# Optimization experiments

Measured on AMD Instinct MI355X. Metric: run time of the kernel, lower is better.

The kernel has to match this reference:

```python
import jax, jax.numpy as jnp
import numpy as np

N, E, D, NUM_REL, NUM_LAYERS = 20000, 100000, 768, 7, 5  # 6 edge types + self-loop relation


def setup_inputs() -> dict:
    key = jax.random.key(0)
    ks = jax.random.split(key, 8)
    x = jax.random.normal(ks[0], (N, D), dtype=jnp.float32)
    edge_index = jax.random.randint(ks[1], (2, E), 0, N, dtype=jnp.int64)
    # original edge_type values are in [-1, 5]; module adds 1 -> [0, 6]
    edge_type = jax.random.randint(ks[2], (E,), -1, 6, dtype=jnp.int64)
    scale = 1.0 / np.sqrt(D)
    weights = jax.random.normal(ks[3], (NUM_LAYERS, NUM_REL, D, D), dtype=jnp.float32) * scale
    roots = jax.random.normal(ks[4], (NUM_LAYERS, D, D), dtype=jnp.float32) * scale
    biases = jax.random.normal(ks[5], (NUM_LAYERS, D), dtype=jnp.float32) * 0.01
    return {"x": x, "edge_index": edge_index, "edge_type": edge_type,
            "weights": weights, "roots": roots, "biases": biases}


def _rgcn_conv(h, src, dst, safe_et, W, root, b):
    # PyG RGCNConv (aggr='mean', root_weight=True, bias=True):
    #   out = x @ root + b + sum_r mean_{edges of rel r into v}(x[src]) @ W_r
    n = h.shape[0]
    hs = h[src]  # [E, D] gather once, reused across relations
    out = h @ root + b
    for r in range(NUM_REL):
        m = (safe_et == r).astype(h.dtype)  # [E]
        msg_sum = jax.ops.segment_sum(hs * m[:, None], dst, num_segments=n)  # [N, D]
        cnt = jax.ops.segment_sum(m, dst, num_segments=n)  # [N]
        mean = msg_sum / jnp.maximum(cnt, 1.0)[:, None]  # zero where no rel-r edges
        out = out + mean @ W[r]
    return out


def reference(x, edge_index, edge_type, weights, roots, biases):
    src, dst = edge_index[0], edge_index[1]
    safe_et = edge_type + 1  # [-1..5] -> [0..6]
    h = x
    for l in range(NUM_LAYERS):
        h = _rgcn_conv(h, src, dst, safe_et, weights[l], roots[l], biases[l])
        h = jax.nn.relu(h)  # dropout=0 -> identity
    return h
```

## Files before the change

kernel.cpp:

```cpp
#include <hip/hip_runtime.h>

typedef unsigned short u16;
typedef unsigned int   u32;
typedef __attribute__((ext_vector_type(8))) short short8;
typedef __attribute__((ext_vector_type(4))) float f32x4;

#define DD      768
#define KK      6144
#define NREL    7
#define NLAYERS 5

__device__ __forceinline__ float b2f(u16 v) {
  return __uint_as_float(((u32)v) << 16);
}
__device__ __forceinline__ u16 f2bf(float f) {
  u32 x = __float_as_uint(f);
  x += 0x7fffu + ((x >> 16) & 1u);
  return (u16)(x >> 16);
}
__device__ __forceinline__ void gload16(const void* g, void* l) {
  __builtin_amdgcn_global_load_lds(
      (const __attribute__((address_space(1))) void*)g,
      (__attribute__((address_space(3))) void*)l, 16, 0, 0);
}


__global__ void cast_x_kernel(const float* __restrict__ x, u16* __restrict__ H, size_t n) {
  for (size_t i = ((size_t)blockIdx.x * 256 + threadIdx.x) * 4; i < n; i += (size_t)gridDim.x * 256 * 4) {
    float4 v = *(const float4*)&x[i];
    u32 lo = (u32)f2bf(v.x) | ((u32)f2bf(v.y) << 16);
    u32 hi = (u32)f2bf(v.z) | ((u32)f2bf(v.w) << 16);
    uint2 o; o.x = lo; o.y = hi;
    *(uint2*)&H[i] = o;
  }
}

__global__ void count_kernel(const int* __restrict__ eidx, const int* __restrict__ etype,
                             int* cnt_dst, int* cnt_rel, int E, int Nn) {
  int e = blockIdx.x * 256 + threadIdx.x;
  if (e >= E) return;
  int dst = eidx[E + e];
  int rel = etype[e] + 1;
  atomicAdd(&cnt_dst[dst], 1);
  atomicAdd(&cnt_rel[(size_t)rel * Nn + dst], 1);
}

__global__ __launch_bounds__(1024) void scan_kernel(const int* __restrict__ cnt, int* __restrict__ offs, int n) {
  __shared__ int part[1024];
  int t = threadIdx.x;
  int per = (n + 1023) / 1024;
  int base = t * per;
  int s = 0;
  for (int i = 0; i < per; ++i) { int idx = base + i; if (idx < n) s += cnt[idx]; }
  part[t] = s;
  __syncthreads();
  for (int o = 1; o < 1024; o <<= 1) {
    int v = (t >= o) ? part[t - o] : 0;
    __syncthreads();
    part[t] += v;
    __syncthreads();
  }
  int excl = (t == 0) ? 0 : part[t - 1];
  s = excl;
  for (int i = 0; i < per; ++i) { int idx = base + i; if (idx < n) { offs[idx] = s; s += cnt[idx]; } }
  if (t == 1023) offs[n] = part[1023];
}

__global__ void fillperm_kernel(const int* __restrict__ eidx, const int* __restrict__ offs,
                                int* fill, int* perm, int E) {
  int e = blockIdx.x * 256 + threadIdx.x;
  if (e >= E) return;
  int dst = eidx[E + e];
  int pos = offs[dst] + atomicAdd(&fill[dst], 1);
  perm[pos] = e;
}

__global__ void wcat_kernel(const float* __restrict__ W, const float* __restrict__ R, u16* __restrict__ Bt) {
  __shared__ float t[32 * 33];
  int b = blockIdx.x;
  int s = b / 576, rem = b % 576;
  int kt = rem / 24, nt = rem % 24;
  const float* src = (s == 0) ? R : (W + (size_t)(s - 1) * DD * DD);
  int tj = threadIdx.x & 31, ti = threadIdx.x >> 5;
#pragma unroll
  for (int i = 0; i < 4; ++i) {
    int kk = kt * 32 + ti + i * 8;
    t[(ti + i * 8) * 33 + tj] = src[(size_t)kk * DD + nt * 32 + tj];
  }
  __syncthreads();
#pragma unroll
  for (int i = 0; i < 4; ++i) {
    int nn_ = nt * 32 + ti + i * 8;
    Bt[(size_t)nn_ * KK + (size_t)s * DD + kt * 32 + tj] = f2bf(t[tj * 33 + ti + i * 8]);
  }
}

__global__ __launch_bounds__(192) void aggregate_kernel(
    const u16* __restrict__ H, const int* __restrict__ esrc, const int* __restrict__ etype,
    const int* __restrict__ offs, const int* __restrict__ perm, const int* __restrict__ cnt_rel,
    u16* __restrict__ Acat, int node0, int Nn) {
  int v = node0 + blockIdx.x;
  int t = threadIdx.x;
  int j0 = t * 4;
  size_t rowbase = (size_t)blockIdx.x * KK;
  *(uint2*)&Acat[rowbase + j0] = *(const uint2*)&H[(size_t)v * DD + j0];
  float a0[4] = {0,0,0,0}, a1[4] = {0,0,0,0}, a2[4] = {0,0,0,0}, a3[4] = {0,0,0,0};
  float a4[4] = {0,0,0,0}, a5[4] = {0,0,0,0}, a6[4] = {0,0,0,0};
  int beg = offs[v], end = offs[v + 1];
  for (int e = beg; e < end; ++e) {
    int eid = perm[e];
    int src = esrc[eid];
    int rel = etype[eid] + 1;
    uint2 w = *(const uint2*)&H[(size_t)src * DD + j0];
    float f0 = b2f((u16)(w.x & 0xffff));
    float f1 = b2f((u16)(w.x >> 16));
    float f2 = b2f((u16)(w.y & 0xffff));
    float f3 = b2f((u16)(w.y >> 16));
    switch (rel) {
      case 0: a0[0]+=f0; a0[1]+=f1; a0[2]+=f2; a0[3]+=f3; break;
      case 1: a1[0]+=f0; a1[1]+=f1; a1[2]+=f2; a1[3]+=f3; break;
      case 2: a2[0]+=f0; a2[1]+=f1; a2[2]+=f2; a2[3]+=f3; break;
      case 3: a3[0]+=f0; a3[1]+=f1; a3[2]+=f2; a3[3]+=f3; break;
      case 4: a4[0]+=f0; a4[1]+=f1; a4[2]+=f2; a4[3]+=f3; break;
      case 5: a5[0]+=f0; a5[1]+=f1; a5[2]+=f2; a5[3]+=f3; break;
      default: a6[0]+=f0; a6[1]+=f1; a6[2]+=f2; a6[3]+=f3; break;
    }
  }
  const float* regs[NREL] = {a0, a1, a2, a3, a4, a5, a6};
#pragma unroll
  for (int r = 0; r < NREL; ++r) {
    int c = cnt_rel[(size_t)r * Nn + v];
    float inv = (c > 0) ? 1.f / (float)c : 0.f;
    const float* a = regs[r];
    u32 lo = (u32)f2bf(a[0] * inv) | ((u32)f2bf(a[1] * inv) << 16);
    u32 hi = (u32)f2bf(a[2] * inv) | ((u32)f2bf(a[3] * inv) << 16);
    uint2 o; o.x = lo; o.y = hi;
    *(uint2*)&Acat[rowbase + (size_t)(r + 1) * DD + j0] = o;
  }
}


#define MFMA_(a_, b_, c_) __builtin_amdgcn_mfma_f32_16x16x32_bf16(a_, b_, c_, 0, 0, 0)

__global__ __launch_bounds__(512, 4) void gemm128_kernel(
    const u16* __restrict__ A, const u16* __restrict__ Bt, const float* __restrict__ bias,
    u16* __restrict__ Hout, float* __restrict__ Cout, int Mvalid, int Mtiles) {
  __shared__ u16 smA[3][128 * 32];
  __shared__ u16 smB[3][256 * 32];

  int tid = threadIdx.x;
  int lane = tid & 63;
  int wv = tid >> 6;
  int wm = wv >> 2, wn = wv & 3;

  int nwg = Mtiles * 3;
  int orig = (int)blockIdx.x;
  int q8 = nwg >> 3, r8 = nwg & 7;
  int xcd = orig & 7, rank = orig >> 3;
  int wg = (xcd < r8 ? xcd * (q8 + 1) : r8 * (q8 + 1) + (xcd - r8) * q8) + rank;
  int bm = wg / 3, bn = wg % 3;

  int srow = tid >> 2;
  int schunk = (tid & 3) ^ ((tid >> 3) & 3);
  int ra = bm * 128 + srow; if (ra > Mvalid - 1) ra = Mvalid - 1;
  const char* gA  = (const char*)A  + (size_t)ra * (KK * 2) + schunk * 16;
  const char* gB0 = (const char*)Bt + (size_t)(bn * 256 + srow) * (KK * 2) + schunk * 16;
  const char* gB1 = gB0 + (size_t)128 * (KK * 2);

  int rsel = lane & 15, kq = lane >> 4;
  int loff = rsel * 64 + ((kq ^ ((rsel >> 1) & 3)) * 16);

  f32x4 acc[4][4];
#pragma unroll
  for (int m = 0; m < 4; ++m)
#pragma unroll
    for (int n = 0; n < 4; ++n) acc[m][n] = (f32x4){0.f, 0.f, 0.f, 0.f};

  const int NSTEP = KK / 32;

#define STAGE(t2, slot)                                                  \
  do {                                                                   \
    size_t ko_ = (size_t)(t2) * 64;                                      \
    gload16(gA + ko_,  (char*)&smA[slot][0] + tid * 16);                 \
    gload16(gB0 + ko_, (char*)&smB[slot][0] + tid * 16);                 \
    gload16(gB1 + ko_, (char*)&smB[slot][0] + 8192 + tid * 16);          \
  } while (0)

#define KSTEP(tt, cur, nxt)                                              \
  do {                                                                   \
    if ((tt) + 2 < NSTEP) STAGE((tt) + 2, nxt);                          \
    const char* aB_ = (const char*)&smA[cur][0] + wm * 4096 + loff;      \
    const char* bB_ = (const char*)&smB[cur][0] + wn * 4096 + loff;      \
    short8 af_[4], bf_[4];                                               \
    _Pragma("unroll")                                                    \
    for (int m_ = 0; m_ < 4; ++m_) af_[m_] = *(const short8*)(aB_ + m_ * 1024); \
    _Pragma("unroll")                                                    \
    for (int n_ = 0; n_ < 4; ++n_) bf_[n_] = *(const short8*)(bB_ + n_ * 1024); \
    __builtin_amdgcn_s_setprio(1);                                       \
    _Pragma("unroll")                                                    \
    for (int m_ = 0; m_ < 4; ++m_)                                       \
      _Pragma("unroll")                                                  \
      for (int n_ = 0; n_ < 4; ++n_)                                     \
        acc[m_][n_] = MFMA_(af_[m_], bf_[n_], acc[m_][n_]);              \
    __builtin_amdgcn_s_setprio(0);                                       \
    if ((tt) + 2 < NSTEP) asm volatile("s_waitcnt vmcnt(3)" ::: "memory"); \
    else                  asm volatile("s_waitcnt vmcnt(0)" ::: "memory"); \
    __builtin_amdgcn_s_barrier();                                        \
  } while (0)

  STAGE(0, 0);
  STAGE(1, 1);
  asm volatile("s_waitcnt vmcnt(3)" ::: "memory");
  __builtin_amdgcn_s_barrier();

  for (int t = 0; t < NSTEP; t += 3) {
    KSTEP(t,     0, 2);
    KSTEP(t + 1, 1, 0);
    KSTEP(t + 2, 2, 1);
  }
#undef KSTEP
#undef STAGE

  int rif = (lane >> 4) * 4;
  int cidx = lane & 15;
#pragma unroll
  for (int m = 0; m < 4; ++m) {
    int rl = bm * 128 + wm * 64 + m * 16 + rif;
#pragma unroll
    for (int n = 0; n < 4; ++n) {
      int c = bn * 256 + wn * 64 + n * 16 + cidx;
      float bv = bias[c];
#pragma unroll
      for (int j = 0; j < 4; ++j) {
        int r = rl + j;
        if (r < Mvalid) {
          float v = acc[m][n][j] + bv;
          v = v > 0.f ? v : 0.f;
          if (Hout) Hout[(size_t)r * DD + c] = f2bf(v);
          if (Cout) Cout[(size_t)r * DD + c] = v;
        }
      }
    }
  }
}


static inline size_t alignup(size_t x, size_t a) { return (x + a - 1) & ~(a - 1); }

extern "C" void kernel_launch(void* const* d_in, const int* in_sizes, int n_in,
                              void* d_out, int out_size, void* d_ws, size_t ws_size,
                              hipStream_t stream) {
  const float* x       = (const float*)d_in[0];
  const int*   eidx    = (const int*)d_in[1];
  const int*   etype   = (const int*)d_in[2];
  const float* weights = (const float*)d_in[3];
  const float* roots   = (const float*)d_in[4];
  const float* biases  = (const float*)d_in[5];
  float* out = (float*)d_out;

  const int Nn = in_sizes[0] / DD;
  const int E  = in_sizes[2];

  char* p = (char*)d_ws;
  size_t off = 0;
  auto carve = [&](size_t bytes) -> char* {
    char* r = p + off;
    off = alignup(off + bytes, 256);
    return r;
  };
  u16* H0      = (u16*)carve((size_t)Nn * DD * 2);
  u16* Bt      = (u16*)carve((size_t)DD * KK * 2);
  int* cnt_rel = (int*)carve((size_t)NREL * Nn * 4);
  int* cnt_dst = (int*)carve((size_t)Nn * 4);
  int* offs    = (int*)carve((size_t)(Nn + 1) * 4);
  int* fill    = (int*)carve((size_t)Nn * 4);
  int* perm    = (int*)carve((size_t)E * 4);

  size_t rem = (ws_size > off) ? (ws_size - off) : 0;
  int McCap = (int)(rem / ((size_t)KK * 2));
  int Mpad = ((Nn + 127) / 128) * 128;
  int Mc = (McCap < Mpad) ? (McCap & ~127) : Mpad;
  if (Mc < 128) return;
  u16* Acat = (u16*)(p + off);
  int nchunks = (Nn + Mc - 1) / Mc;
  u16* H1 = (u16*)d_out;

  (void)hipMemsetAsync(cnt_rel, 0, (size_t)NREL * Nn * 4, stream);
  (void)hipMemsetAsync(cnt_dst, 0, (size_t)Nn * 4, stream);
  (void)hipMemsetAsync(fill, 0, (size_t)Nn * 4, stream);

  int eg = (E + 255) / 256;
  count_kernel<<<eg, 256, 0, stream>>>(eidx, etype, cnt_dst, cnt_rel, E, Nn);
  scan_kernel<<<1, 1024, 0, stream>>>(cnt_dst, offs, Nn);
  fillperm_kernel<<<eg, 256, 0, stream>>>(eidx, offs, fill, perm, E);
  cast_x_kernel<<<2048, 256, 0, stream>>>(x, H0, (size_t)Nn * DD);

  const u16* Hin = H0;
  u16* Hnext = H1;
  for (int l = 0; l < NLAYERS; ++l) {
    wcat_kernel<<<8 * 576, 256, 0, stream>>>(weights + (size_t)l * NREL * DD * DD,
                                             roots + (size_t)l * DD * DD, Bt);
    for (int c = 0; c < nchunks; ++c) {
      int node0 = c * Mc;
      int nn = (Nn - node0 < Mc) ? (Nn - node0) : Mc;
      aggregate_kernel<<<nn, 192, 0, stream>>>(Hin, eidx, etype, offs, perm, cnt_rel,
                                               Acat, node0, Nn);
      int mt = (nn + 127) / 128;
      u16* ho = (l < NLAYERS - 1) ? (Hnext + (size_t)node0 * DD) : nullptr;
      float* co = (l == NLAYERS - 1) ? (out + (size_t)node0 * DD) : nullptr;
      gemm128_kernel<<<mt * 3, 512, 0, stream>>>(Acat, Bt, biases + (size_t)l * DD, ho, co, nn, mt);
    }
    const u16* t_ = Hin;
    Hin = Hnext;
    Hnext = (u16*)t_;
  }
}
```

Measured before the change: 1.583 ms.

## Pre-tile A and B into MFMA fragment layout and load fragments directly without LDS

Result: slower. 2.423 ms (+53.1%).

```diff
diff --git a/kernel.cpp b/kernel.cpp
--- a/kernel.cpp
+++ b/kernel.cpp
@@ -9,6 +9,7 @@
 #define KK      6144
 #define NREL    7
 #define NLAYERS 5
+#define TILEB   196608
 
 __device__ __forceinline__ float b2f(u16 v) {
   return __uint_as_float(((u32)v) << 16);
@@ -17,11 +18,6 @@
   u32 x = __float_as_uint(f);
   x += 0x7fffu + ((x >> 16) & 1u);
   return (u16)(x >> 16);
-}
-__device__ __forceinline__ void gload16(const void* g, void* l) {
-  __builtin_amdgcn_global_load_lds(
-      (const __attribute__((address_space(1))) void*)g,
-      (__attribute__((address_space(3))) void*)l, 16, 0, 0);
 }
 
 
@@ -75,7 +71,7 @@
   perm[pos] = e;
 }
 
-__global__ void wcat_kernel(const float* __restrict__ W, const float* __restrict__ R, u16* __restrict__ Bt) {
+__global__ void wcat_kernel(const float* __restrict__ W, const float* __restrict__ R, u16* __restrict__ Bn) {
   __shared__ float t[32 * 33];
   int b = blockIdx.x;
   int s = b / 576, rem = b % 576;
@@ -88,27 +84,35 @@
     t[(ti + i * 8) * 33 + tj] = src[(size_t)kk * DD + nt * 32 + tj];
   }
   __syncthreads();
+  int kkidx = s * 24 + kt;
+  int kq = tj >> 3, e = tj & 7;
 #pragma unroll
   for (int i = 0; i < 4; ++i) {
-    int nn_ = nt * 32 + ti + i * 8;
-    Bt[(size_t)nn_ * KK + (size_t)s * DD + kt * 32 + tj] = f2bf(t[tj * 33 + ti + i * 8]);
+    int n = nt * 32 + ti + i * 8;
+    size_t idx = ((size_t)(n >> 4) * 192 + kkidx) * 512 + (size_t)(kq * 16 + (n & 15)) * 8 + e;
+    Bn[idx] = f2bf(t[tj * 33 + ti + i * 8]);
   }
 }
 
 __global__ __launch_bounds__(192) void aggregate_kernel(
     const u16* __restrict__ H, const int* __restrict__ esrc, const int* __restrict__ etype,
     const int* __restrict__ offs, const int* __restrict__ perm, const int* __restrict__ cnt_rel,
-    u16* __restrict__ Acat, int node0, int Nn) {
+    u16* __restrict__ An, int node0, int Nn) {
   int v = node0 + blockIdx.x;
   int t = threadIdx.x;
   int j0 = t * 4;
-  size_t rowbase = (size_t)blockIdx.x * KK;
-  *(uint2*)&Acat[rowbase + j0] = *(const uint2*)&H[(size_t)v * DD + j0];
+  int rr = blockIdx.x;
+  int tile16 = rr >> 4, rsel = rr & 15;
+  int kq = (j0 & 31) >> 3, e = j0 & 7, kk0 = j0 >> 5;
+  size_t base = ((size_t)tile16 * 192 + kk0) * 512 + (size_t)(kq * 16 + rsel) * 8 + e;
+
+  *(uint2*)&An[base] = *(const uint2*)&H[(size_t)v * DD + j0];
+
   float a0[4] = {0,0,0,0}, a1[4] = {0,0,0,0}, a2[4] = {0,0,0,0}, a3[4] = {0,0,0,0};
   float a4[4] = {0,0,0,0}, a5[4] = {0,0,0,0}, a6[4] = {0,0,0,0};
   int beg = offs[v], end = offs[v + 1];
-  for (int e = beg; e < end; ++e) {
-    int eid = perm[e];
+  for (int eI = beg; eI < end; ++eI) {
+    int eid = perm[eI];
     int src = esrc[eid];
     int rel = etype[eid] + 1;
     uint2 w = *(const uint2*)&H[(size_t)src * DD + j0];
@@ -135,100 +139,86 @@
     u32 lo = (u32)f2bf(a[0] * inv) | ((u32)f2bf(a[1] * inv) << 16);
     u32 hi = (u32)f2bf(a[2] * inv) | ((u32)f2bf(a[3] * inv) << 16);
     uint2 o; o.x = lo; o.y = hi;
-    *(uint2*)&Acat[rowbase + (size_t)(r + 1) * DD + j0] = o;
+    *(uint2*)&An[base + (size_t)(r + 1) * 24 * 512] = o;
   }
 }
 
 
 #define MFMA_(a_, b_, c_) __builtin_amdgcn_mfma_f32_16x16x32_bf16(a_, b_, c_, 0, 0, 0)
 
-__global__ __launch_bounds__(512, 4) void gemm128_kernel(
-    const u16* __restrict__ A, const u16* __restrict__ Bt, const float* __restrict__ bias,
+__global__ __launch_bounds__(256, 2) void gemmfl_kernel(
+    const u16* __restrict__ An, const u16* __restrict__ Bn, const float* __restrict__ bias,
     u16* __restrict__ Hout, float* __restrict__ Cout, int Mvalid, int Mtiles) {
-  __shared__ u16 smA[3][128 * 32];
-  __shared__ u16 smB[3][256 * 32];
-
   int tid = threadIdx.x;
   int lane = tid & 63;
   int wv = tid >> 6;
-  int wm = wv >> 2, wn = wv & 3;
 
   int nwg = Mtiles * 3;
   int orig = (int)blockIdx.x;
   int q8 = nwg >> 3, r8 = nwg & 7;
   int xcd = orig & 7, rank = orig >> 3;
   int wg = (xcd < r8 ? xcd * (q8 + 1) : r8 * (q8 + 1) + (xcd - r8) * q8) + rank;
-  int bm = wg / 3, bn = wg % 3;
-
-  int srow = tid >> 2;
-  int schunk = (tid & 3) ^ ((tid >> 3) & 3);
-  int ra = bm * 128 + srow; if (ra > Mvalid - 1) ra = Mvalid - 1;
-  const char* gA  = (const char*)A  + (size_t)ra * (KK * 2) + schunk * 16;
-  const char* gB0 = (const char*)Bt + (size_t)(bn * 256 + srow) * (KK * 2) + schunk * 16;
-  const char* gB1 = gB0 + (size_t)128 * (KK * 2);
-
-  int rsel = lane & 15, kq = lane >> 4;
-  int loff = rsel * 64 + ((kq ^ ((rsel >> 1) & 3)) * 16);
-
-  f32x4 acc[4][4];
-#pragma unroll
-  for (int m = 0; m < 4; ++m)
+  int bm = wg / 3, bq = wg % 3;
+  int nq = bq * 4 + wv;
+
+  const char* pa = (const char*)An + (size_t)(bm * 8) * TILEB;
+  const char* pb = (const char*)Bn + (size_t)(nq * 4) * TILEB;
+  int voff = lane * 16;
+
+  f32x4 acc[8][4];
+#pragma unroll
+  for (int m = 0; m < 8; ++m)
 #pragma unroll
     for (int n = 0; n < 4; ++n) acc[m][n] = (f32x4){0.f, 0.f, 0.f, 0.f};
 
-  const int NSTEP = KK / 32;
-
-#define STAGE(t2, slot)                                                  \
-  do {                                                                   \
-    size_t ko_ = (size_t)(t2) * 64;                                      \
-    gload16(gA + ko_,  (char*)&smA[slot][0] + tid * 16);                 \
-    gload16(gB0 + ko_, (char*)&smB[slot][0] + tid * 16);                 \
-    gload16(gB1 + ko_, (char*)&smB[slot][0] + 8192 + tid * 16);          \
+#define LOADK(kk, ar, br)                                                 \
+  do {                                                                    \
+    int o_ = (kk) * 1024 + voff;                                          \
+    _Pragma("unroll")                                                     \
+    for (int m_ = 0; m_ < 8; ++m_) ar[m_] = *(const short8*)(pa + m_ * TILEB + o_); \
+    _Pragma("unroll")                                                     \
+    for (int n_ = 0; n_ < 4; ++n_) br[n_] = *(const short8*)(pb + n_ * TILEB + o_); \
   } while (0)
 
-#define KSTEP(tt, cur, nxt)                                              \
-  do {                                                                   \
-    if ((tt) + 2 < NSTEP) STAGE((tt) + 2, nxt);                          \
-    const char* aB_ = (const char*)&smA[cur][0] + wm * 4096 + loff;      \
-    const char* bB_ = (const char*)&smB[cur][0] + wn * 4096 + loff;      \
-    short8 af_[4], bf_[4];                                               \
-    _Pragma("unroll")                                                    \
-    for (int m_ = 0; m_ < 4; ++m_) af_[m_] = *(const short8*)(aB_ + m_ * 1024); \
-    _Pragma("unroll")                                                    \
-    for (int n_ = 0; n_ < 4; ++n_) bf_[n_] = *(const short8*)(bB_ + n_ * 1024); \
-    __builtin_amdgcn_s_setprio(1);                                       \
-    _Pragma("unroll")                                                    \
-    for (int m_ = 0; m_ < 4; ++m_)                                       \
-      _Pragma("unroll")                                                  \
-      for (int n_ = 0; n_ < 4; ++n_)                                     \
-        acc[m_][n_] = MFMA_(af_[m_], bf_[n_], acc[m_][n_]);              \
-    __builtin_amdgcn_s_setprio(0);                                       \
-    if ((tt) + 2 < NSTEP) asm volatile("s_waitcnt vmcnt(3)" ::: "memory"); \
-    else                  asm volatile("s_waitcnt vmcnt(0)" ::: "memory"); \
-    __builtin_amdgcn_s_barrier();                                        \
+#define MF32(ar, br)                                                      \
+  do {                                                                    \
+    __builtin_amdgcn_s_setprio(1);                                        \
+    _Pragma("unroll")                                                     \
+    for (int m_ = 0; m_ < 8; ++m_)                                        \
+      _Pragma("unroll")                                                   \
+      for (int n_ = 0; n_ < 4; ++n_)                                      \
+        acc[m_][n_] = MFMA_(ar[m_], br[n_], acc[m_][n_]);                 \
+    __builtin_amdgcn_s_setprio(0);                                        \
   } while (0)
 
-  STAGE(0, 0);
-  STAGE(1, 1);
-  asm volatile("s_waitcnt vmcnt(3)" ::: "memory");
-  __builtin_amdgcn_s_barrier();
-
-  for (int t = 0; t < NSTEP; t += 3) {
-    KSTEP(t,     0, 2);
-    KSTEP(t + 1, 1, 0);
-    KSTEP(t + 2, 2, 1);
-  }
-#undef KSTEP
-#undef STAGE
+  short8 aA[8], bA[4], aB[8], bB[4];
+  LOADK(0, aA, bA);
+  LOADK(1, aB, bB);
+
+  for (int kk = 0; kk < 188; kk += 2) {
+    MF32(aA, bA);
+    LOADK(kk + 2, aA, bA);
+    MF32(aB, bB);
+    LOADK(kk + 3, aB, bB);
+  }
+  MF32(aA, bA);
+  LOADK(190, aA, bA);
+  MF32(aB, bB);
+  LOADK(191, aB, bB);
+  MF32(aA, bA);
+  MF32(aB, bB);
+
+#undef LOADK
+#undef MF32
 
   int rif = (lane >> 4) * 4;
   int cidx = lane & 15;
 #pragma unroll
-  for (int m = 0; m < 4; ++m) {
-    int rl = bm * 128 + wm * 64 + m * 16 + rif;
+  for (int m = 0; m < 8; ++m) {
+    int rl = bm * 128 + m * 16 + rif;
 #pragma unroll
     for (int n = 0; n < 4; ++n) {
-      int c = bn * 256 + wn * 64 + n * 16 + cidx;
+      int c = nq * 64 + n * 16 + cidx;
       float bv = bias[c];
 #pragma unroll
       for (int j = 0; j < 4; ++j) {
@@ -269,7 +259,7 @@
     return r;
   };
   u16* H0      = (u16*)carve((size_t)Nn * DD * 2);
-  u16* Bt      = (u16*)carve((size_t)DD * KK * 2);
+  u16* Bn      = (u16*)carve((size_t)DD * KK * 2);
   int* cnt_rel = (int*)carve((size_t)NREL * Nn * 4);
   int* cnt_dst = (int*)carve((size_t)Nn * 4);
   int* offs    = (int*)carve((size_t)(Nn + 1) * 4);
@@ -281,7 +271,7 @@
   int Mpad = ((Nn + 127) / 128) * 128;
   int Mc = (McCap < Mpad) ? (McCap & ~127) : Mpad;
   if (Mc < 128) return;
-  u16* Acat = (u16*)(p + off);
+  u16* An = (u16*)(p + off);
   int nchunks = (Nn + Mc - 1) / Mc;
   u16* H1 = (u16*)d_out;
 
@@ -299,16 +289,16 @@
   u16* Hnext = H1;
   for (int l = 0; l < NLAYERS; ++l) {
     wcat_kernel<<<8 * 576, 256, 0, stream>>>(weights + (size_t)l * NREL * DD * DD,
-                                             roots + (size_t)l * DD * DD, Bt);
+                                             roots + (size_t)l * DD * DD, Bn);
     for (int c = 0; c < nchunks; ++c) {
       int node0 = c * Mc;
       int nn = (Nn - node0 < Mc) ? (Nn - node0) : Mc;
       aggregate_kernel<<<nn, 192, 0, stream>>>(Hin, eidx, etype, offs, perm, cnt_rel,
-                                               Acat, node0, Nn);
+                                               An, node0, Nn);
       int mt = (nn + 127) / 128;
       u16* ho = (l < NLAYERS - 1) ? (Hnext + (size_t)node0 * DD) : nullptr;
       float* co = (l == NLAYERS - 1) ? (out + (size_t)node0 * DD) : nullptr;
-      gemm128_kernel<<<mt * 3, 512, 0, stream>>>(Acat, Bt, biases + (size_t)l * DD, ho, co, nn, mt);
+      gemmfl_kernel<<<mt * 3, 256, 0, stream>>>(An, Bn, biases + (size_t)l * DD, ho, co, nn, mt);
     }
     const u16* t_ = Hin;
     Hin = Hnext;
```

## Replace GEMM with 256x256-tile eight-phase pipelined MFMA kernel

Applied to the files above, without the earlier changes.

After: 1.430 ms. 9.6% less time.

```diff
diff --git a/kernel.cpp b/kernel.cpp
--- a/kernel.cpp
+++ b/kernel.cpp
@@ -141,12 +141,20 @@
 
 
 #define MFMA_(a_, b_, c_) __builtin_amdgcn_mfma_f32_16x16x32_bf16(a_, b_, c_, 0, 0, 0)
-
-__global__ __launch_bounds__(512, 4) void gemm128_kernel(
+#define BAR   __builtin_amdgcn_s_barrier()
+#define SB    __builtin_amdgcn_sched_barrier(0)
+#define LGKM0 asm volatile("s_waitcnt lgkmcnt(0)" ::: "memory")
+#define VM10  asm volatile("s_waitcnt vmcnt(10)" ::: "memory")
+#define VM8   asm volatile("s_waitcnt vmcnt(8)" ::: "memory")
+#define VM4   asm volatile("s_waitcnt vmcnt(4)" ::: "memory")
+#define VM2   asm volatile("s_waitcnt vmcnt(2)" ::: "memory")
+#define VM0   asm volatile("s_waitcnt vmcnt(0)" ::: "memory")
+
+__global__ __launch_bounds__(512, 2) void gemm8p_kernel(
     const u16* __restrict__ A, const u16* __restrict__ Bt, const float* __restrict__ bias,
     u16* __restrict__ Hout, float* __restrict__ Cout, int Mvalid, int Mtiles) {
-  __shared__ u16 smA[3][128 * 32];
-  __shared__ u16 smB[3][256 * 32];
+  __shared__ char smA[2][2][16384];
+  __shared__ char smB[2][2][16384];
 
   int tid = threadIdx.x;
   int lane = tid & 63;
@@ -160,72 +168,125 @@
   int wg = (xcd < r8 ? xcd * (q8 + 1) : r8 * (q8 + 1) + (xcd - r8) * q8) + rank;
   int bm = wg / 3, bn = wg % 3;
 
-  int srow = tid >> 2;
-  int schunk = (tid & 3) ^ ((tid >> 3) & 3);
-  int ra = bm * 128 + srow; if (ra > Mvalid - 1) ra = Mvalid - 1;
-  const char* gA  = (const char*)A  + (size_t)ra * (KK * 2) + schunk * 16;
-  const char* gB0 = (const char*)Bt + (size_t)(bn * 256 + srow) * (KK * 2) + schunk * 16;
-  const char* gB1 = gB0 + (size_t)128 * (KK * 2);
-
+  const char* pA[2][2];
+  const char* pB[2][2];
+#pragma unroll
+  for (int j = 0; j < 2; ++j) {
+    int q = j * 512 + tid, rl = q >> 3, gc = (q & 7) ^ (rl & 7);
+    int ra0 = (rl & 63) + ((rl >> 6) << 7);
+    int rb0 = (rl & 31) + ((rl >> 5) << 6);
+    pA[0][j] = (const char*)A  + ((size_t)(bm * 256 + ra0) * KK) * 2 + gc * 16;
+    pA[1][j] = pA[0][j] + (size_t)64 * KK * 2;
+    pB[0][j] = (const char*)Bt + ((size_t)(bn * 256 + rb0) * KK) * 2 + gc * 16;
+    pB[1][j] = pB[0][j] + (size_t)32 * KK * 2;
+  }
   int rsel = lane & 15, kq = lane >> 4;
-  int loff = rsel * 64 + ((kq ^ ((rsel >> 1) & 3)) * 16);
-
-  f32x4 acc[4][4];
-#pragma unroll
-  for (int m = 0; m < 4; ++m)
+  int loff0 = rsel * 128 + (((kq)     ^ (rsel & 7)) * 16);
+  int loff1 = rsel * 128 + (((kq + 4) ^ (rsel & 7)) * 16);
+
+  f32x4 acc[8][4];
+#pragma unroll
+  for (int m = 0; m < 8; ++m)
 #pragma unroll
     for (int n = 0; n < 4; ++n) acc[m][n] = (f32x4){0.f, 0.f, 0.f, 0.f};
 
-  const int NSTEP = KK / 32;
-
-#define STAGE(t2, slot)                                                  \
-  do {                                                                   \
-    size_t ko_ = (size_t)(t2) * 64;                                      \
-    gload16(gA + ko_,  (char*)&smA[slot][0] + tid * 16);                 \
-    gload16(gB0 + ko_, (char*)&smB[slot][0] + tid * 16);                 \
-    gload16(gB1 + ko_, (char*)&smB[slot][0] + 8192 + tid * 16);          \
+  short8 a03[4][2], a47[4][2], b01[2][2], b23[2][2];
+
+#define STGA(s_, h_, t2)                                                  \
+  do {                                                                    \
+    size_t ko_ = (size_t)(t2) * 128;                                      \
+    gload16(pA[h_][0] + ko_, &smA[s_][h_][0] + tid * 16);                 \
+    gload16(pA[h_][1] + ko_, &smA[s_][h_][8192] + tid * 16);              \
   } while (0)
-
-#define KSTEP(tt, cur, nxt)                                              \
-  do {                                                                   \
-    if ((tt) + 2 < NSTEP) STAGE((tt) + 2, nxt);                          \
-    const char* aB_ = (const char*)&smA[cur][0] + wm * 4096 + loff;      \
-    const char* bB_ = (const char*)&smB[cur][0] + wn * 4096 + loff;      \
-    short8 af_[4], bf_[4];                                               \
-    _Pragma("unroll")                                                    \
-    for (int m_ = 0; m_ < 4; ++m_) af_[m_] = *(const short8*)(aB_ + m_ * 1024); \
-    _Pragma("unroll")                                                    \
-    for (int n_ = 0; n_ < 4; ++n_) bf_[n_] = *(const short8*)(bB_ + n_ * 1024); \
-    __builtin_amdgcn_s_setprio(1);                                       \
-    _Pragma("unroll")                                                    \
-    for (int m_ = 0; m_ < 4; ++m_)                                       \
-      _Pragma("unroll")                                                  \
-      for (int n_ = 0; n_ < 4; ++n_)                                     \
-        acc[m_][n_] = MFMA_(af_[m_], bf_[n_], acc[m_][n_]);              \
-    __builtin_amdgcn_s_setprio(0);                                       \
-    if ((tt) + 2 < NSTEP) asm volatile("s_waitcnt vmcnt(3)" ::: "memory"); \
-    else                  asm volatile("s_waitcnt vmcnt(0)" ::: "memory"); \
-    __builtin_amdgcn_s_barrier();                                        \
+#define STGB(s_, h_, t2)                                                  \
+  do {                                                                    \
+    size_t ko_ = (size_t)(t2) * 128;                                      \
+    gload16(pB[h_][0] + ko_, &smB[s_][h_][0] + tid * 16);                 \
+    gload16(pB[h_][1] + ko_, &smB[s_][h_][8192] + tid * 16);              \
   } while (0)
 
-  STAGE(0, 0);
-  STAGE(1, 1);
-  asm volatile("s_waitcnt vmcnt(3)" ::: "memory");
-  __builtin_amdgcn_s_barrier();
-
-  for (int t = 0; t < NSTEP; t += 3) {
-    KSTEP(t,     0, 2);
-    KSTEP(t + 1, 1, 0);
-    KSTEP(t + 2, 2, 1);
-  }
-#undef KSTEP
-#undef STAGE
+#define Q_(accm, accn, AR, BR)                                            \
+  acc[accm][accn] = MFMA_(AR[0], BR[0], acc[accm][accn]);                 \
+  acc[accm][accn] = MFMA_(AR[1], BR[1], acc[accm][accn]);
+
+#define TILE(s_, S1, S2, S3, S4, V1, V2, V4)                              \
+  do {                                                                    \
+                     \
+    _Pragma("unroll")                                                     \
+    for (int m = 0; m < 4; ++m) {                                         \
+      a03[m][0] = *(const short8*)(&smA[s_][0][0] + (wm * 64 + m * 16) * 128 + loff0); \
+      a03[m][1] = *(const short8*)(&smA[s_][0][0] + (wm * 64 + m * 16) * 128 + loff1); \
+    }                                                                     \
+    _Pragma("unroll")                                                     \
+    for (int n = 0; n < 2; ++n) {                                         \
+      b01[n][0] = *(const short8*)(&smB[s_][0][0] + (wn * 32 + n * 16) * 128 + loff0); \
+      b01[n][1] = *(const short8*)(&smB[s_][0][0] + (wn * 32 + n * 16) * 128 + loff1); \
+    }                                                                     \
+    S1;                                                                   \
+    asm volatile("s_waitcnt lgkmcnt(8)" ::: "memory");                    \
+    BAR; LGKM0; SB;                                                       \
+    __builtin_amdgcn_s_setprio(1);                                        \
+    _Pragma("unroll")                                                     \
+    for (int m = 0; m < 4; ++m) { Q_(m, 0, a03[m], b01[0]); Q_(m, 1, a03[m], b01[1]); } \
+    __builtin_amdgcn_s_setprio(0);                                        \
+    V1; BAR; SB;                                                          \
+                          \
+    _Pragma("unroll")                                                     \
+    for (int m = 0; m < 4; ++m) {                                         \
+      a47[m][0] = *(const short8*)(&smA[s_][1][0] + (wm * 64 + m * 16) * 128 + loff0); \
+      a47[m][1] = *(const short8*)(&smA[s_][1][0] + (wm * 64 + m * 16) * 128 + loff1); \
+    }                                                                     \
+    S2;                                                                   \
+    BAR; LGKM0; SB;                                                       \
+    __builtin_amdgcn_s_setprio(1);                                        \
+    _Pragma("unroll")                                                     \
+    for (int m = 0; m < 4; ++m) { Q_(m + 4, 0, a47[m], b01[0]); Q_(m + 4, 1, a47[m], b01[1]); } \
+    __builtin_amdgcn_s_setprio(0);                                        \
+    V2; BAR; SB;                                                          \
+                          \
+    _Pragma("unroll")                                                     \
+    for (int n = 0; n < 2; ++n) {                                         \
+      b23[n][0] = *(const short8*)(&smB[s_][1][0] + (wn * 32 + n * 16) * 128 + loff0); \
+      b23[n][1] = *(const short8*)(&smB[s_][1][0] + (wn * 32 + n * 16) * 128 + loff1); \
+    }                                                                     \
+    S3;                                                                   \
+    BAR; LGKM0; SB;                                                       \
+    __builtin_amdgcn_s_setprio(1);                                        \
+    _Pragma("unroll")                                                     \
+    for (int m = 0; m < 4; ++m) { Q_(m + 4, 2, a47[m], b23[0]); Q_(m + 4, 3, a47[m], b23[1]); } \
+    __builtin_amdgcn_s_setprio(0);                                        \
+    BAR; SB;                                                              \
+                              \
+    S4;                                                                   \
+    BAR; SB;                                                              \
+    __builtin_amdgcn_s_setprio(1);                                        \
+    _Pragma("unroll")                                                     \
+    for (int m = 0; m < 4; ++m) { Q_(m, 2, a03[m], b23[0]); Q_(m, 3, a03[m], b23[1]); } \
+    __builtin_amdgcn_s_setprio(0);                                        \
+    V4; BAR; SB;                                                          \
+  } while (0)
+
+  STGA(0, 0, 0); STGB(0, 0, 0); STGA(0, 1, 0); STGB(0, 1, 0);
+  STGA(1, 0, 1); STGB(1, 0, 1); STGA(1, 1, 1);
+  VM10; BAR; SB;
+
+  for (int t = 0; t < 94; t += 2) {
+    TILE(0, STGB(1, 1, t + 1), STGA(0, 0, t + 2), STGB(0, 0, t + 2), STGA(0, 1, t + 2), VM10, VM10, VM10);
+    TILE(1, STGB(0, 1, t + 2), STGA(1, 0, t + 3), STGB(1, 0, t + 3), STGA(1, 1, t + 3), VM10, VM10, VM10);
+  }
+  TILE(0, STGB(1, 1, 95), , , , VM10, VM8, VM4);
+  TILE(1, , , , , VM2, VM0, );
+
+#undef TILE
+#undef Q_
+#undef STGA
+#undef STGB
 
   int rif = (lane >> 4) * 4;
   int cidx = lane & 15;
 #pragma unroll
-  for (int m = 0; m < 4; ++m) {
-    int rl = bm * 128 + wm * 64 + m * 16 + rif;
+  for (int m = 0; m < 8; ++m) {
+    int rl = bm * 256 + wm * 128 + m * 16 + rif;
 #pragma unroll
     for (int n = 0; n < 4; ++n) {
       int c = bn * 256 + wn * 64 + n * 16 + cidx;
@@ -278,9 +339,9 @@
 
   size_t rem = (ws_size > off) ? (ws_size - off) : 0;
   int McCap = (int)(rem / ((size_t)KK * 2));
-  int Mpad = ((Nn + 127) / 128) * 128;
-  int Mc = (McCap < Mpad) ? (McCap & ~127) : Mpad;
-  if (Mc < 128) return;
+  int Mpad = ((Nn + 255) / 256) * 256;
+  int Mc = (McCap < Mpad) ? (McCap & ~255) : Mpad;
+  if (Mc < 256) return;
   u16* Acat = (u16*)(p + off);
   int nchunks = (Nn + Mc - 1) / Mc;
   u16* H1 = (u16*)d_out;
@@ -305,10 +366,10 @@
       int nn = (Nn - node0 < Mc) ? (Nn - node0) : Mc;
       aggregate_kernel<<<nn, 192, 0, stream>>>(Hin, eidx, etype, offs, perm, cnt_rel,
                                                Acat, node0, Nn);
-      int mt = (nn + 127) / 128;
+      int mt = (nn + 255) / 256;
       u16* ho = (l < NLAYERS - 1) ? (Hnext + (size_t)node0 * DD) : nullptr;
       float* co = (l == NLAYERS - 1) ? (out + (size_t)node0 * DD) : nullptr;
-      gemm128_kernel<<<mt * 3, 512, 0, stream>>>(Acat, Bt, biases + (size_t)l * DD, ho, co, nn, mt);
+      gemm8p_kernel<<<mt * 3, 512, 0, stream>>>(Acat, Bt, biases + (size_t)l * DD, ho, co, nn, mt);
     }
     const u16* t_ = Hin;
     Hin = Hnext;
```

## Switch GEMM to 256x256 tiles with 4 waves and register double-buffered fragments

Applied to the files above, without the earlier changes.

Result: slower. 1.653 ms (+4.4%).

```diff
diff --git a/kernel.cpp b/kernel.cpp
--- a/kernel.cpp
+++ b/kernel.cpp
@@ -141,17 +141,21 @@
 
 
 #define MFMA_(a_, b_, c_) __builtin_amdgcn_mfma_f32_16x16x32_bf16(a_, b_, c_, 0, 0, 0)
-
-__global__ __launch_bounds__(512, 4) void gemm128_kernel(
+#define BAR   __builtin_amdgcn_s_barrier()
+#define SCB   __builtin_amdgcn_sched_barrier(0)
+#define VM8   asm volatile("s_waitcnt vmcnt(8)" ::: "memory")
+#define VM0   asm volatile("s_waitcnt vmcnt(0)" ::: "memory")
+
+__global__ __launch_bounds__(256, 1) void gemm4w_kernel(
     const u16* __restrict__ A, const u16* __restrict__ Bt, const float* __restrict__ bias,
     u16* __restrict__ Hout, float* __restrict__ Cout, int Mvalid, int Mtiles) {
-  __shared__ u16 smA[3][128 * 32];
-  __shared__ u16 smB[3][256 * 32];
+  __shared__ char smA[4][16384];
+  __shared__ char smB[4][16384];
 
   int tid = threadIdx.x;
   int lane = tid & 63;
   int wv = tid >> 6;
-  int wm = wv >> 2, wn = wv & 3;
+  int wm = wv >> 1, wn = wv & 1;
 
   int nwg = Mtiles * 3;
   int orig = (int)blockIdx.x;
@@ -161,74 +165,98 @@
   int bm = wg / 3, bn = wg % 3;
 
   int srow = tid >> 2;
-  int schunk = (tid & 3) ^ ((tid >> 3) & 3);
-  int ra = bm * 128 + srow; if (ra > Mvalid - 1) ra = Mvalid - 1;
-  const char* gA  = (const char*)A  + (size_t)ra * (KK * 2) + schunk * 16;
-  const char* gB0 = (const char*)Bt + (size_t)(bn * 256 + srow) * (KK * 2) + schunk * 16;
-  const char* gB1 = gB0 + (size_t)128 * (KK * 2);
-
+  int sch = (tid & 3) ^ ((tid >> 3) & 3);
+  const char* gA[4];
+  const char* gB[4];
+#pragma unroll
+  for (int j = 0; j < 4; ++j) {
+    int ra = bm * 256 + j * 64 + srow;
+    if (ra > Mvalid - 1) ra = Mvalid - 1;
+    gA[j] = (const char*)A  + (size_t)ra * (KK * 2) + sch * 16;
+    gB[j] = (const char*)Bt + (size_t)(bn * 256 + j * 64 + srow) * (KK * 2) + sch * 16;
+  }
   int rsel = lane & 15, kq = lane >> 4;
   int loff = rsel * 64 + ((kq ^ ((rsel >> 1) & 3)) * 16);
 
-  f32x4 acc[4][4];
-#pragma unroll
-  for (int m = 0; m < 4; ++m)
-#pragma unroll
-    for (int n = 0; n < 4; ++n) acc[m][n] = (f32x4){0.f, 0.f, 0.f, 0.f};
-
-  const int NSTEP = KK / 32;
-
-#define STAGE(t2, slot)                                                  \
-  do {                                                                   \
-    size_t ko_ = (size_t)(t2) * 64;                                      \
-    gload16(gA + ko_,  (char*)&smA[slot][0] + tid * 16);                 \
-    gload16(gB0 + ko_, (char*)&smB[slot][0] + tid * 16);                 \
-    gload16(gB1 + ko_, (char*)&smB[slot][0] + 8192 + tid * 16);          \
+  f32x4 acc[8][8];
+#pragma unroll
+  for (int m = 0; m < 8; ++m)
+#pragma unroll
+    for (int n = 0; n < 8; ++n) acc[m][n] = (f32x4){0.f, 0.f, 0.f, 0.f};
+
+#define STAGE(st, s_)                                                     \
+  do {                                                                    \
+    size_t ko_ = (size_t)(st) * 64;                                       \
+    gload16(gA[0] + ko_, &smA[s_][tid * 16]);                             \
+    gload16(gA[1] + ko_, &smA[s_][4096 + tid * 16]);                      \
+    gload16(gA[2] + ko_, &smA[s_][8192 + tid * 16]);                      \
+    gload16(gA[3] + ko_, &smA[s_][12288 + tid * 16]);                     \
+    gload16(gB[0] + ko_, &smB[s_][tid * 16]);                             \
+    gload16(gB[1] + ko_, &smB[s_][4096 + tid * 16]);                      \
+    gload16(gB[2] + ko_, &smB[s_][8192 + tid * 16]);                      \
+    gload16(gB[3] + ko_, &smB[s_][12288 + tid * 16]);                     \
   } while (0)
 
-#define KSTEP(tt, cur, nxt)                                              \
-  do {                                                                   \
-    if ((tt) + 2 < NSTEP) STAGE((tt) + 2, nxt);                          \
-    const char* aB_ = (const char*)&smA[cur][0] + wm * 4096 + loff;      \
-    const char* bB_ = (const char*)&smB[cur][0] + wn * 4096 + loff;      \
-    short8 af_[4], bf_[4];                                               \
-    _Pragma("unroll")                                                    \
-    for (int m_ = 0; m_ < 4; ++m_) af_[m_] = *(const short8*)(aB_ + m_ * 1024); \
-    _Pragma("unroll")                                                    \
-    for (int n_ = 0; n_ < 4; ++n_) bf_[n_] = *(const short8*)(bB_ + n_ * 1024); \
-    __builtin_amdgcn_s_setprio(1);                                       \
-    _Pragma("unroll")                                                    \
-    for (int m_ = 0; m_ < 4; ++m_)                                       \
-      _Pragma("unroll")                                                  \
-      for (int n_ = 0; n_ < 4; ++n_)                                     \
-        acc[m_][n_] = MFMA_(af_[m_], bf_[n_], acc[m_][n_]);              \
-    __builtin_amdgcn_s_setprio(0);                                       \
-    if ((tt) + 2 < NSTEP) asm volatile("s_waitcnt vmcnt(3)" ::: "memory"); \
-    else                  asm volatile("s_waitcnt vmcnt(0)" ::: "memory"); \
-    __builtin_amdgcn_s_barrier();                                        \
+#define READF(s_, AR, BR)                                                 \
+  do {                                                                    \
+    _Pragma("unroll")                                                     \
+    for (int m_ = 0; m_ < 8; ++m_)                                        \
+      AR[m_] = *(const short8*)(&smA[s_][(wm * 128 + m_ * 16) * 64 + loff]); \
+    _Pragma("unroll")                                                     \
+    for (int n_ = 0; n_ < 8; ++n_)                                        \
+      BR[n_] = *(const short8*)(&smB[s_][(wn * 128 + n_ * 16) * 64 + loff]); \
   } while (0)
+
+#define MFMA64(AR, BR)                                                    \
+  do {                                                                    \
+    _Pragma("unroll")                                                     \
+    for (int m_ = 0; m_ < 8; ++m_)                                        \
+      _Pragma("unroll")                                                   \
+      for (int n_ = 0; n_ < 8; ++n_)                                      \
+        acc[m_][n_] = MFMA_(AR[m_], BR[n_], acc[m_][n_]);                 \
+  } while (0)
+
+#define HALF(sSt, sSl, rSl, RA, RB, MA, MB)                               \
+  do {                                                                    \
+    STAGE(sSt, sSl);                                                      \
+    VM8; BAR; SCB;                                                        \
+    READF(rSl, RA, RB);                                                   \
+    MFMA64(MA, MB);                                                       \
+  } while (0)
+
+  short8 aE[8], bE[8], aO[8], bO[8];
 
   STAGE(0, 0);
   STAGE(1, 1);
-  asm volatile("s_waitcnt vmcnt(3)" ::: "memory");
-  __builtin_amdgcn_s_barrier();
-
-  for (int t = 0; t < NSTEP; t += 3) {
-    KSTEP(t,     0, 2);
-    KSTEP(t + 1, 1, 0);
-    KSTEP(t + 2, 2, 1);
-  }
-#undef KSTEP
+  VM8; BAR; SCB;
+  READF(0, aE, bE);
+
+  for (int t = 0; t < 188; t += 4) {
+    HALF(t + 2, 2, 1, aO, bO, aE, bE);
+    HALF(t + 3, 3, 2, aE, bE, aO, bO);
+    HALF(t + 4, 0, 3, aO, bO, aE, bE);
+    HALF(t + 5, 1, 0, aE, bE, aO, bO);
+  }
+  HALF(190, 2, 1, aO, bO, aE, bE);
+  HALF(191, 3, 2, aE, bE, aO, bO);
+  VM0; BAR; SCB;
+  READF(3, aO, bO);
+  MFMA64(aE, bE);
+  MFMA64(aO, bO);
+
+#undef HALF
+#undef MFMA64
+#undef READF
 #undef STAGE
 
   int rif = (lane >> 4) * 4;
   int cidx = lane & 15;
 #pragma unroll
-  for (int m = 0; m < 4; ++m) {
-    int rl = bm * 128 + wm * 64 + m * 16 + rif;
-#pragma unroll
-    for (int n = 0; n < 4; ++n) {
-      int c = bn * 256 + wn * 64 + n * 16 + cidx;
+  for (int m = 0; m < 8; ++m) {
+    int rl = bm * 256 + wm * 128 + m * 16 + rif;
+#pragma unroll
+    for (int n = 0; n < 8; ++n) {
+      int c = bn * 256 + wn * 128 + n * 16 + cidx;
       float bv = bias[c];
 #pragma unroll
       for (int j = 0; j < 4; ++j) {
@@ -278,9 +306,9 @@
 
   size_t rem = (ws_size > off) ? (ws_size - off) : 0;
   int McCap = (int)(rem / ((size_t)KK * 2));
-  int Mpad = ((Nn + 127) / 128) * 128;
-  int Mc = (McCap < Mpad) ? (McCap & ~127) : Mpad;
-  if (Mc < 128) return;
+  int Mpad = ((Nn + 255) / 256) * 256;
+  int Mc = (McCap < Mpad) ? (McCap & ~255) : Mpad;
+  if (Mc < 256) return;
   u16* Acat = (u16*)(p + off);
   int nchunks = (Nn + Mc - 1) / Mc;
   u16* H1 = (u16*)d_out;
@@ -305,10 +333,10 @@
       int nn = (Nn - node0 < Mc) ? (Nn - node0) : Mc;
       aggregate_kernel<<<nn, 192, 0, stream>>>(Hin, eidx, etype, offs, perm, cnt_rel,
                                                Acat, node0, Nn);
-      int mt = (nn + 127) / 128;
+      int mt = (nn + 255) / 256;
       u16* ho = (l < NLAYERS - 1) ? (Hnext + (size_t)node0 * DD) : nullptr;
       float* co = (l == NLAYERS - 1) ? (out + (size_t)node0 * DD) : nullptr;
-      gemm128_kernel<<<mt * 3, 512, 0, stream>>>(Acat, Bt, biases + (size_t)l * DD, ho, co, nn, mt);
+      gemm4w_kernel<<<mt * 3, 256, 0, stream>>>(Acat, Bt, biases + (size_t)l * DD, ho, co, nn, mt);
     }
     const u16* t_ = Hin;
     Hin = Hnext;
```
